# Kernel tuning notes

Measured on AMD Instinct MI355X. Metric: run time of the kernel, lower is better.

## Reference

```python
import jax, jax.numpy as jnp
import numpy as np

NEG_SLOPE = 0.01  # F.leaky_relu default
EPS = 1e-6


def setup_inputs() -> dict:
    key = jax.random.key(0)
    k1, k2, k3, k4 = jax.random.split(key, 4)
    N, E, IN, OUT = 100000, 1600000, 128, 64
    x = jax.random.normal(k1, (N, IN), dtype=jnp.float32)
    W = jax.random.normal(k2, (OUT, IN), dtype=jnp.float32) * (1.0 / np.sqrt(IN))
    a = jax.random.uniform(k3, (2 * OUT,), dtype=jnp.float32)  # uniform [0,1) as in init
    edge_index = jax.random.randint(k4, (2, E), 0, N, dtype=jnp.int64)
    return {"x": x, "W": W, "a": a, "edge_index": edge_index}


def reference(x, W, a, edge_index):
    N = x.shape[0]
    out_f = W.shape[0]
    # add self loops: append (i, i) for every node
    loops = jnp.arange(N, dtype=edge_index.dtype)
    ei = jnp.concatenate([edge_index, jnp.stack([loops, loops])], axis=1)
    src, dst = ei[0], ei[1]

    messages = x @ W.T                      # [N, out]
    h_src = messages[src]                   # [E', out]
    h_dst = messages[dst]                   # [E', out]

    # e = cat([h_dst, h_src]) . a  == h_dst.a[:out] + h_src.a[out:]
    e = h_dst @ a[:out_f] + h_src @ a[out_f:]
    e = jnp.where(e >= 0, e, NEG_SLOPE * e)  # leaky_relu
    w = jnp.exp(e)                           # unnormalized edge weights

    denom = jax.ops.segment_sum(w, dst, num_segments=N)                     # [N]
    agg = jax.ops.segment_sum(h_src * w[:, None], dst, num_segments=N)      # [N, out]
    return agg / jnp.clip(denom, EPS)[:, None]
```

## Files before the change

kernel.cpp:

```cpp
#include <hip/hip_runtime.h>
#include <hip/hip_bf16.h>

#define IN_F 128
#define OUT_F 64
#define NEG 0.01f
#define LDSP 132
#define WTP  68

#define BUCKET_N 256
#define EPB 8192
#define CAP 48
#define MAXB 512
#define MAXSLAB 512

__device__ __forceinline__ float leaky_exp(float e) {
    e = (e >= 0.f) ? e : NEG * e;
    return expf(e);
}

__device__ __forceinline__ float b2f(unsigned int v) { return __uint_as_float(v); }

__global__ __launch_bounds__(256) void gemm_msg_kernel(
    const float* __restrict__ x, const float* __restrict__ W,
    const float* __restrict__ a,
    __hip_bfloat16* __restrict__ msg, float2* __restrict__ ab, int N)
{
    __shared__ float xs[64 * LDSP];
    __shared__ float Wt[IN_F * WTP];
    const int tid = threadIdx.x;
    const int base = blockIdx.x * 64;

#pragma unroll
    for (int t = 0; t < 8; ++t) {
        int i = tid + t * 256;
        int o = i & 63;
        int k4 = i >> 6;
        float4 wv = ((const float4*)W)[o * (IN_F / 4) + k4];
        Wt[(k4 * 4 + 0) * WTP + o] = wv.x;
        Wt[(k4 * 4 + 1) * WTP + o] = wv.y;
        Wt[(k4 * 4 + 2) * WTP + o] = wv.z;
        Wt[(k4 * 4 + 3) * WTP + o] = wv.w;
    }
#pragma unroll
    for (int t = 0; t < 8; ++t) {
        int i = tid + t * 256;
        int r = i >> 5, k4 = i & 31;
        int row = base + r;
        float4 xv = make_float4(0.f, 0.f, 0.f, 0.f);
        if (row < N) xv = ((const float4*)x)[(size_t)row * (IN_F / 4) + k4];
        *(float4*)&xs[r * LDSP + k4 * 4] = xv;
    }
    __syncthreads();

    const int tx = tid & 15;
    const int ty = tid >> 4;
    const float* xrow = &xs[(ty * 4) * LDSP];

    float acc[4][4] = {};
    for (int k = 0; k < IN_F; k += 4) {
        float xq[4][4], wq[4][4];
#pragma unroll
        for (int i = 0; i < 4; ++i)
            *(float4*)xq[i] = *(const float4*)&xrow[i * LDSP + k];
#pragma unroll
        for (int j = 0; j < 4; ++j)
            *(float4*)wq[j] = *(const float4*)&Wt[(k + j) * WTP + tx * 4];
#pragma unroll
        for (int ri = 0; ri < 4; ++ri)
#pragma unroll
            for (int ci = 0; ci < 4; ++ci) {
                acc[ri][ci] += xq[ri][0] * wq[0][ci];
                acc[ri][ci] += xq[ri][1] * wq[1][ci];
                acc[ri][ci] += xq[ri][2] * wq[2][ci];
                acc[ri][ci] += xq[ri][3] * wq[3][ci];
            }
    }

    float a_lo[4], a_hi[4];
#pragma unroll
    for (int ci = 0; ci < 4; ++ci) {
        a_lo[ci] = a[tx * 4 + ci];
        a_hi[ci] = a[OUT_F + tx * 4 + ci];
    }

#pragma unroll
    for (int ri = 0; ri < 4; ++ri) {
        int row = base + ty * 4 + ri;
        if (row < N) {
            union { ushort4 u; __hip_bfloat16 h[4]; } pk;
            pk.h[0] = __float2bfloat16(acc[ri][0]);
            pk.h[1] = __float2bfloat16(acc[ri][1]);
            pk.h[2] = __float2bfloat16(acc[ri][2]);
            pk.h[3] = __float2bfloat16(acc[ri][3]);
            *(ushort4*)&msg[(size_t)row * OUT_F + tx * 4] = pk.u;
        }
        float pa = acc[ri][0] * a_lo[0] + acc[ri][1] * a_lo[1] +
                   acc[ri][2] * a_lo[2] + acc[ri][3] * a_lo[3];
        float pb = acc[ri][0] * a_hi[0] + acc[ri][1] * a_hi[1] +
                   acc[ri][2] * a_hi[2] + acc[ri][3] * a_hi[3];
#pragma unroll
        for (int off = 1; off < 16; off <<= 1) {
            pa += __shfl_xor(pa, off);
            pb += __shfl_xor(pb, off);
        }
        if (tx == 0 && row < N) ab[row] = make_float2(pa, pb);
    }
}

__global__ __launch_bounds__(512) void partition_kernel(
    const int* __restrict__ src, const int* __restrict__ dst,
    int* __restrict__ counts, unsigned int* __restrict__ cells,
    int* __restrict__ bucket_tot, int E, int B, int NBLKP)
{
    __shared__ int cnt_s[MAXB];
    for (int i = threadIdx.x; i < B; i += 512) cnt_s[i] = 0;
    __syncthreads();

    const size_t pbase = (size_t)blockIdx.x * B;

#pragma unroll
    for (int u = 0; u < 4; ++u) {
        const int i4 = blockIdx.x * 2048 + u * 512 + threadIdx.x;
        const int e0 = i4 * 4;
        if (e0 + 3 < E) {
            int4 s4 = ((const int4*)src)[i4];
            int4 d4 = ((const int4*)dst)[i4];
            int b0 = d4.x >> 8, b1 = d4.y >> 8, b2 = d4.z >> 8, b3 = d4.w >> 8;
            int r0 = atomicAdd(&cnt_s[b0], 1);
            int r1 = atomicAdd(&cnt_s[b1], 1);
            int r2 = atomicAdd(&cnt_s[b2], 1);
            int r3 = atomicAdd(&cnt_s[b3], 1);
            if (r0 < CAP) cells[(pbase + b0) * CAP + r0] =
                (unsigned)s4.x | ((unsigned)(d4.x & 255) << 20);
            if (r1 < CAP) cells[(pbase + b1) * CAP + r1] =
                (unsigned)s4.y | ((unsigned)(d4.y & 255) << 20);
            if (r2 < CAP) cells[(pbase + b2) * CAP + r2] =
                (unsigned)s4.z | ((unsigned)(d4.z & 255) << 20);
            if (r3 < CAP) cells[(pbase + b3) * CAP + r3] =
                (unsigned)s4.w | ((unsigned)(d4.w & 255) << 20);
        } else {
            for (int e = e0; e < E && e < e0 + 4; ++e) {
                int s = src[e], d = dst[e];
                int b = d >> 8;
                int r = atomicAdd(&cnt_s[b], 1);
                if (r < CAP) cells[(pbase + b) * CAP + r] =
                    (unsigned)s | ((unsigned)(d & 255) << 20);
            }
        }
    }
    __syncthreads();
    for (int i = threadIdx.x; i < B; i += 512) {
        int c = min(cnt_s[i], CAP);
        counts[(size_t)i * NBLKP + blockIdx.x] = c;
        atomicAdd(&bucket_tot[i], c);
    }
}

__global__ __launch_bounds__(512) void bucket_scan_kernel(
    const int* __restrict__ bucket_tot, int* __restrict__ bucket_base,
    int* __restrict__ offs, int N, int B)
{
    __shared__ int tmp[512];
    const int t = threadIdx.x;
    int v = 0;
    if (t < B) {
        int nodes = N - t * BUCKET_N;
        nodes = max(0, min(BUCKET_N, nodes));
        v = bucket_tot[t] + nodes;
    }
    tmp[t] = v;
    __syncthreads();
#pragma unroll
    for (int d = 1; d < 512; d <<= 1) {
        int add = (t >= d) ? tmp[t - d] : 0;
        __syncthreads();
        tmp[t] += add;
        __syncthreads();
    }
    if (t < B) bucket_base[t] = tmp[t] - v;
    if (t == 511) offs[N] = tmp[511];
}

__global__ __launch_bounds__(512) void compact_kernel(
    const int* __restrict__ counts, const unsigned int* __restrict__ cells,
    const int* __restrict__ bucket_base, const float2* __restrict__ ab,
    int* __restrict__ offs, int2* __restrict__ edges,
    int N, int B, int NBLK, int NBLKP)
{
    __shared__ int cnt_l[MAXSLAB];
    __shared__ int hist[BUCKET_N];
    __shared__ int scan_s[BUCKET_N];
    __shared__ int cursor[BUCKET_N];
    __shared__ float alpha_s[BUCKET_N];
    const int b = blockIdx.x;
    const int tid = threadIdx.x;
    const int wave = tid >> 6, lane = tid & 63;

    for (int i = tid; i < NBLK; i += 512) cnt_l[i] = counts[(size_t)b * NBLKP + i];
    float2 myab = make_float2(0.f, 0.f);
    if (tid < BUCKET_N) {
        int g = b * BUCKET_N + tid;
        bool valid = (g < N);
        hist[tid] = valid ? 1 : 0;
        if (valid) myab = ab[g];
        alpha_s[tid] = myab.x;
    }
    __syncthreads();

    for (int sl = wave; sl < NBLK; sl += 8) {
        int c = cnt_l[sl];
        if (lane < c) {
            unsigned v = cells[((size_t)sl * B + b) * CAP + lane];
            atomicAdd(&hist[v >> 20], 1);
        }
    }
    __syncthreads();

    int hv = 0;
    if (tid < BUCKET_N) { hv = hist[tid]; scan_s[tid] = hv; }
    __syncthreads();
#pragma unroll
    for (int d = 1; d < BUCKET_N; d <<= 1) {
        int add = (tid < BUCKET_N && tid >= d) ? scan_s[tid - d] : 0;
        __syncthreads();
        if (tid < BUCKET_N) scan_s[tid] += add;
        __syncthreads();
    }
    const int gbase = bucket_base[b];
    if (tid < BUCKET_N) {
        int excl = scan_s[tid] - hv;
        int g = b * BUCKET_N + tid;
        if (g < N) {
            offs[g] = gbase + excl;
            float wself = leaky_exp(myab.x + myab.y);
            edges[gbase + excl] = make_int2(g, __float_as_int(wself));
            cursor[tid] = excl + 1;
        }
    }
    __syncthreads();

    for (int sl = wave; sl < NBLK; sl += 8) {
        int c = cnt_l[sl];
        if (lane < c) {
            unsigned v = cells[((size_t)sl * B + b) * CAP + lane];
            int s = v & 0xFFFFF;
            int l = v >> 20;
            float w = leaky_exp(alpha_s[l] + ab[s].y);
            int pos = atomicAdd(&cursor[l], 1);
            edges[gbase + pos] = make_int2(s, __float_as_int(w));
        }
    }
}

__global__ __launch_bounds__(256) void aggregate_kernel(
    const int* __restrict__ offs, const int2* __restrict__ edges,
    const __hip_bfloat16* __restrict__ msg,
    float* __restrict__ out, int N)
{
    const int node = blockIdx.x * 4 + (threadIdx.x >> 6);
    if (node >= N) return;
    const int lane = threadIdx.x & 63;
    const int g = lane & 15;
    const int u = lane >> 4;

    const unsigned short* msp = (const unsigned short*)msg;

    float acc0 = 0.f, acc1 = 0.f, acc2 = 0.f, acc3 = 0.f, den = 0.f;

    const int st = offs[node], en = offs[node + 1];
    for (int j = st; j < en; j += 16) {
#pragma unroll
        for (int uu = 0; uu < 4; ++uu) {
            int idx = j + uu * 4 + u;
            int ii = min(idx, en - 1);
            int2 e = edges[ii];
            float w = (idx < en) ? __int_as_float(e.y) : 0.f;
            ushort4 mv = *(const ushort4*)&msp[(size_t)e.x * OUT_F + 4 * g];
            acc0 += w * b2f((unsigned)mv.x << 16);
            acc1 += w * b2f((unsigned)mv.y << 16);
            acc2 += w * b2f((unsigned)mv.z << 16);
            acc3 += w * b2f((unsigned)mv.w << 16);
            den  += w;
        }
    }

#pragma unroll
    for (int off = 16; off <= 32; off <<= 1) {
        acc0 += __shfl_xor(acc0, off);
        acc1 += __shfl_xor(acc1, off);
        acc2 += __shfl_xor(acc2, off);
        acc3 += __shfl_xor(acc3, off);
        den  += __shfl_xor(den, off);
    }

    if (lane < 16) {
        float dn = 1.f / fmaxf(den, 1e-6f);
        *(float4*)&out[(size_t)node * OUT_F + 4 * lane] =
            make_float4(acc0 * dn, acc1 * dn, acc2 * dn, acc3 * dn);
    }
}

extern "C" void kernel_launch(void* const* d_in, const int* in_sizes, int n_in,
                              void* d_out, int out_size, void* d_ws, size_t ws_size,
                              hipStream_t stream) {
    const float* x  = (const float*)d_in[0];
    const float* W  = (const float*)d_in[1];
    const float* a  = (const float*)d_in[2];
    const int*   ei = (const int*)d_in[3];
    float* out = (float*)d_out;

    const int IN = in_sizes[1] / OUT_F;
    const int N  = in_sizes[0] / IN;
    const int E  = in_sizes[3] / 2;
    const int B  = (N + BUCKET_N - 1) / BUCKET_N;
    const int NBLK  = (E + EPB - 1) / EPB;
    const int NBLKP = (NBLK + 3) & ~3;

    auto align16 = [](size_t v) { return (v + 15) & ~(size_t)15; };
    char* p = (char*)d_ws;
    __hip_bfloat16* msg = (__hip_bfloat16*)p; p += align16((size_t)N * OUT_F * 2);
    float2* ab    = (float2*)p; p += align16((size_t)N * 8);
    int*   counts = (int*)p;   p += align16((size_t)B * NBLKP * 4);
    unsigned int* cells = (unsigned int*)p; p += align16((size_t)NBLK * B * CAP * 4);
    int*   btot   = (int*)p;   p += align16((size_t)B * 4);
    int*   bbase  = (int*)p;   p += align16((size_t)B * 4);
    int*   offs   = (int*)p;   p += align16((size_t)(N + 1) * 4);
    int2*  edges  = (int2*)p;  p += align16((size_t)(E + N) * 8);

    const int* esrc = ei;
    const int* edst = ei + E;

    hipMemsetAsync(btot, 0, (size_t)B * 4, stream);

    gemm_msg_kernel<<<(N + 63) / 64, 256, 0, stream>>>(x, W, a, msg, ab, N);
    partition_kernel<<<NBLK, 512, 0, stream>>>(esrc, edst, counts, cells,
                                               btot, E, B, NBLKP);
    bucket_scan_kernel<<<1, 512, 0, stream>>>(btot, bbase, offs, N, B);
    compact_kernel<<<B, 512, 0, stream>>>(counts, cells, bbase, ab,
                                          offs, edges, N, B, NBLK, NBLKP);
    aggregate_kernel<<<(N + 3) / 4, 256, 0, stream>>>(offs, edges, msg, out, N);
}
```

Baseline: 153.9 us.

## Cache bucket cells in registers across passes and software-pipeline edge loads in aggregate

In the bucket-sort kernel, each wave now keeps its cell words in a register array of up to 32 entries during the histogram pass and reuses them in the scatter pass, so global cells are not read a second time. Slabs beyond that cap still take the old path. The aggregate kernel's 16-edge unrolled loop is replaced by a 4-edge-per-iteration loop that prefetches the next edge record while processing the current one. This raises register pressure in the sort kernel and gives up the wider unroll in aggregation, which may reduce memory-level parallelism.

After: 152.6 us. No clear change (-0.9%).

```diff
diff --git a/kernel.cpp b/kernel.cpp
--- a/kernel.cpp
+++ b/kernel.cpp
@@ -12,6 +12,7 @@
 #define CAP 48
 #define MAXB 512
 #define MAXSLAB 512
+#define CMAXIT 32
 
 __device__ __forceinline__ float leaky_exp(float e) {
     e = (e >= 0.f) ? e : NEG * e;
@@ -207,7 +208,21 @@
     }
     __syncthreads();
 
-    for (int sl = wave; sl < NBLK; sl += 8) {
+    unsigned cell_c[CMAXIT];
+#pragma unroll
+    for (int it = 0; it < CMAXIT; ++it) {
+        int sl = wave + it * 8;
+        unsigned v = 0xFFFFFFFFu;
+        if (sl < NBLK) {
+            int c = cnt_l[sl];
+            if (lane < c) {
+                v = cells[((size_t)sl * B + b) * CAP + lane];
+                atomicAdd(&hist[v >> 20], 1);
+            }
+        }
+        cell_c[it] = v;
+    }
+    for (int sl = wave + CMAXIT * 8; sl < NBLK; sl += 8) {
         int c = cnt_l[sl];
         if (lane < c) {
             unsigned v = cells[((size_t)sl * B + b) * CAP + lane];
@@ -239,12 +254,23 @@
     }
     __syncthreads();
 
-    for (int sl = wave; sl < NBLK; sl += 8) {
+#pragma unroll
+    for (int it = 0; it < CMAXIT; ++it) {
+        unsigned v = cell_c[it];
+        if (v != 0xFFFFFFFFu) {
+            int s = v & 0xFFFFF;
+            int l = (v >> 20) & 255;
+            float w = leaky_exp(alpha_s[l] + ab[s].y);
+            int pos = atomicAdd(&cursor[l], 1);
+            edges[gbase + pos] = make_int2(s, __float_as_int(w));
+        }
+    }
+    for (int sl = wave + CMAXIT * 8; sl < NBLK; sl += 8) {
         int c = cnt_l[sl];
         if (lane < c) {
             unsigned v = cells[((size_t)sl * B + b) * CAP + lane];
             int s = v & 0xFFFFF;
-            int l = v >> 20;
+            int l = (v >> 20) & 255;
             float w = leaky_exp(alpha_s[l] + ab[s].y);
             int pos = atomicAdd(&cursor[l], 1);
             edges[gbase + pos] = make_int2(s, __float_as_int(w));
@@ -268,20 +294,21 @@
     float acc0 = 0.f, acc1 = 0.f, acc2 = 0.f, acc3 = 0.f, den = 0.f;
 
     const int st = offs[node], en = offs[node + 1];
-    for (int j = st; j < en; j += 16) {
-#pragma unroll
-        for (int uu = 0; uu < 4; ++uu) {
-            int idx = j + uu * 4 + u;
-            int ii = min(idx, en - 1);
-            int2 e = edges[ii];
-            float w = (idx < en) ? __int_as_float(e.y) : 0.f;
-            ushort4 mv = *(const ushort4*)&msp[(size_t)e.x * OUT_F + 4 * g];
-            acc0 += w * b2f((unsigned)mv.x << 16);
-            acc1 += w * b2f((unsigned)mv.y << 16);
-            acc2 += w * b2f((unsigned)mv.z << 16);
-            acc3 += w * b2f((unsigned)mv.w << 16);
-            den  += w;
-        }
+
+    int idx = st + u;
+    int2 e = edges[min(idx, en - 1)];
+    for (int j = st; j < en; j += 4) {
+        const int nidx = idx + 4;
+        const int2 enx = edges[min(nidx, en - 1)];
+        const float w = (idx < en) ? __int_as_float(e.y) : 0.f;
+        const ushort4 mv = *(const ushort4*)&msp[(size_t)e.x * OUT_F + 4 * g];
+        acc0 += w * b2f((unsigned)mv.x << 16);
+        acc1 += w * b2f((unsigned)mv.y << 16);
+        acc2 += w * b2f((unsigned)mv.z << 16);
+        acc3 += w * b2f((unsigned)mv.w << 16);
+        den  += w;
+        idx = nidx;
+        e = enx;
     }
 
 #pragma unroll
```
